# Kernel optimization log

Measured on AMD Instinct MI355X. Metric: run time of the kernel, lower is better.

The kernel has to match this reference:

```python
import jax, jax.numpy as jnp
import numpy as np

N = 100000
E = 1600000
IN_DIM = 128
HID = 64
NCOMM = 32


def setup_inputs() -> dict:
    key = jax.random.key(0)
    k = jax.random.split(key, 8)
    x = jax.random.normal(k[0], (N, IN_DIM), dtype=jnp.float32)
    edge_index = jax.random.randint(k[1], (2, E), 0, N, dtype=jnp.int64)
    s1 = 1.0 / np.sqrt(IN_DIM)
    s2 = 1.0 / np.sqrt(HID)
    W1 = jax.random.uniform(k[2], (IN_DIM, HID), jnp.float32, -s1, s1)
    b1 = jnp.zeros((HID,), jnp.float32)
    W2 = jax.random.uniform(k[3], (HID, HID), jnp.float32, -s2, s2)
    b2 = jnp.zeros((HID,), jnp.float32)
    Wfc = jax.random.uniform(k[4], (HID, NCOMM), jnp.float32, -s2, s2)
    bfc = jax.random.uniform(k[5], (NCOMM,), jnp.float32, -s2, s2)
    return {"x": x, "edge_index": edge_index, "W1": W1, "b1": b1,
            "W2": W2, "b2": b2, "Wfc": Wfc, "bfc": bfc}


def gcn_conv(x, row, col, norm, W, b):
    # PyG GCNConv: linear -> gather(source) * norm -> scatter_add(target) -> + bias
    h = x @ W                                    # [N, out]
    msgs = h[row] * norm[:, None]                # [E+N, out] gather (memory-bound)
    agg = jax.ops.segment_sum(msgs, col, num_segments=x.shape[0])
    return agg + b


def reference(x, edge_index, W1, b1, W2, b2, Wfc, bfc):
    n = x.shape[0]
    # add self-loops (PyG GCNConv default)
    loop = jnp.arange(n, dtype=edge_index.dtype)
    row = jnp.concatenate([edge_index[0], loop])  # source
    col = jnp.concatenate([edge_index[1], loop])  # target
    # symmetric normalization D^{-1/2} (A+I) D^{-1/2}
    deg = jax.ops.segment_sum(jnp.ones_like(col, dtype=x.dtype), col, num_segments=n)
    dinv = jnp.where(deg > 0, jax.lax.rsqrt(deg), 0.0)
    norm = dinv[row] * dinv[col]
    h = jax.nn.relu(gcn_conv(x, row, col, norm, W1, b1))   # dropout = identity (eval)
    h = jax.nn.relu(gcn_conv(h, row, col, norm, W2, b2))
    return jax.nn.sigmoid(h @ Wfc + bfc)
```

## Files before the change

### kernel.cpp

```cpp
#include <hip/hip_runtime.h>
#include <hip/hip_fp16.h>
#include <math.h>

#define N_NODES 100000
#define N_EDGES 1600000
#define IN_DIM  128
#define HID     64
#define NCOMM   32
#define NB        391
#define BSHIFT    8
#define EPB       4096
#define NBIN_BLK  391

typedef _Float16 f16x8 __attribute__((ext_vector_type(8)));
typedef float    f32x4 __attribute__((ext_vector_type(4)));

__global__ void k_detect(const unsigned int* __restrict__ e, int* __restrict__ flag) {
  int lane = threadIdx.x;
  unsigned v = 0;
  #pragma unroll
  for (int i = 0; i < 4; ++i) v |= e[2 * (lane * 4 + i) + 1];
  unsigned long long nz = __ballot(v != 0u);
  if (lane == 0) *flag = (nz == 0ull) ? 1 : 0;
}

__device__ __forceinline__ int load_idx(const int* e32, long long pos, int is64) {
  if (is64) return (int)(((const long long*)e32)[pos]);
  return e32[pos];
}

__global__ __launch_bounds__(256) void k_bhist(const int* __restrict__ e, int* __restrict__ bcnt,
                                               const int* __restrict__ flag) {
  __shared__ int cnt[NB];
  for (int i = threadIdx.x; i < NB; i += 256) cnt[i] = 0;
  __syncthreads();
  int is64 = *flag;
  long long base = (long long)blockIdx.x * EPB;
  #pragma unroll
  for (int j = 0; j < EPB / 256; ++j) {
    long long eid = base + j * 256 + threadIdx.x;
    if (eid < N_EDGES) {
      int c = load_idx(e, (long long)N_EDGES + eid, is64);
      atomicAdd(&cnt[c >> BSHIFT], 1);
    }
  }
  __syncthreads();
  for (int b = threadIdx.x; b < NB; b += 256)
    if (cnt[b]) atomicAdd(&bcnt[b], cnt[b]);
}

__global__ __launch_bounds__(512) void k_bscan(const int* __restrict__ bcnt, int* __restrict__ bptr,
                                               int* __restrict__ bcur) {
  __shared__ int sm[512];
  int t = threadIdx.x;
  int v = (t < NB) ? bcnt[t] : 0;
  sm[t] = v;
  __syncthreads();
  for (int off = 1; off < 512; off <<= 1) {
    int u = (t >= off) ? sm[t - off] : 0;
    __syncthreads();
    sm[t] += u;
    __syncthreads();
  }
  if (t < NB) {
    int ex = sm[t] - v;
    bptr[t] = ex;
    bcur[t] = ex;
  }
  if (t == 0) bptr[NB] = N_EDGES;
}

__global__ __launch_bounds__(256) void k_bin(const int* __restrict__ e, int* __restrict__ bcur,
                                             uint2* __restrict__ ebuf, const int* __restrict__ flag) {
  __shared__ int cnt[NB];
  __shared__ int base[NB];
  for (int i = threadIdx.x; i < NB; i += 256) cnt[i] = 0;
  __syncthreads();
  int is64 = *flag;
  long long eb = (long long)blockIdx.x * EPB;
  int rr[EPB / 256], cc[EPB / 256], lr[EPB / 256];
  #pragma unroll
  for (int j = 0; j < EPB / 256; ++j) {
    long long eid = eb + j * 256 + threadIdx.x;
    if (eid < N_EDGES) {
      rr[j] = load_idx(e, eid, is64);
      cc[j] = load_idx(e, (long long)N_EDGES + eid, is64);
      lr[j] = atomicAdd(&cnt[cc[j] >> BSHIFT], 1);
    }
  }
  __syncthreads();
  for (int b = threadIdx.x; b < NB; b += 256)
    base[b] = cnt[b] ? atomicAdd(&bcur[b], cnt[b]) : 0;
  __syncthreads();
  #pragma unroll
  for (int j = 0; j < EPB / 256; ++j) {
    long long eid = eb + j * 256 + threadIdx.x;
    if (eid < N_EDGES) {
      int pos = base[cc[j] >> BSHIFT] + lr[j];
      ebuf[pos] = make_uint2((unsigned)rr[j], (unsigned)cc[j]);
    }
  }
}

__global__ __launch_bounds__(256) void k_deg(const uint2* __restrict__ ebuf, const int* __restrict__ bptr,
                                             float* __restrict__ dinv, int* __restrict__ ptr) {
  __shared__ int cnt[256];
  __shared__ int scn[256];
  int t = threadIdx.x;
  int b = blockIdx.x;
  int c0 = b << BSHIFT;
  cnt[t] = 0;
  __syncthreads();
  int s = bptr[b], epos = bptr[b + 1];
  for (int i = s + t; i < epos; i += 256)
    atomicAdd(&cnt[(int)ebuf[i].y - c0], 1);
  __syncthreads();
  int d = cnt[t];
  scn[t] = d;
  __syncthreads();
  for (int off = 1; off < 256; off <<= 1) {
    int u = (t >= off) ? scn[t - off] : 0;
    __syncthreads();
    scn[t] += u;
    __syncthreads();
  }
  int node = c0 + t;
  if (node < N_NODES) {
    dinv[node] = rsqrtf((float)d + 1.0f);
    ptr[node] = bptr[b] + scn[t] - d;
  }
  if (b == NB - 1 && t == 0) ptr[N_NODES] = N_EDGES;
}

__global__ __launch_bounds__(1024) void k_fsort(const uint2* __restrict__ ebuf, const int* __restrict__ bptr,
                                                const int* __restrict__ ptr, const float* __restrict__ dinv,
                                                uint2* __restrict__ pk) {
  __shared__ int cur[256];
  int b = blockIdx.x;
  int c0 = b << BSHIFT;
  if (threadIdx.x < 256) {
    int node = c0 + threadIdx.x;
    cur[threadIdx.x] = (node < N_NODES) ? ptr[node] : 0;
  }
  __syncthreads();
  int s = bptr[b], epos = bptr[b + 1];
  for (int i = s + (int)threadIdx.x; i < epos; i += 1024) {
    uint2 ed = ebuf[i];
    int r = (int)ed.x, c = (int)ed.y;
    float w = dinv[r] * dinv[c];
    int pos = atomicAdd(&cur[c - c0], 1);
    pk[pos] = make_uint2((unsigned)r, __float_as_uint(w));
  }
}

template<int K, int M, bool FINAL, bool INH>
__global__ __launch_bounds__(256) void k_mfma(const void* __restrict__ X, const float* __restrict__ W,
                                              void* __restrict__ Y, const float* __restrict__ bias) {
  constexpr int NN = M / 16;
  constexpr int KS = K / 32;
  __shared__ char smem[M * K * 2];

  const int tid = threadIdx.x;
  for (int i = tid; i < K * M / 4; i += 256) {
    int k  = i / (M / 4);
    int mf = (i % (M / 4)) * 4;
    float4 wv = *(const float4*)(W + (size_t)k * M + mf);
    float wa[4] = {wv.x, wv.y, wv.z, wv.w};
    #pragma unroll
    for (int c = 0; c < 4; ++c) {
      int m = mf + c;
      int byte_off = m * (2 * K) + ((((k >> 3) << 4)) ^ ((m & 7) << 4)) + (k & 7) * 2;
      *(_Float16*)(smem + byte_off) = (_Float16)wa[c];
    }
  }
  __syncthreads();

  const int lane = tid & 63;
  const int wv_  = tid >> 6;
  const int rowbase = blockIdx.x * 128 + wv_ * 32;
  const int lr = lane & 15;
  const int kg = lane >> 4;
  const int r0 = rowbase + lr;
  const int r1 = r0 + 16;
  const int rc0 = (r0 < N_NODES) ? r0 : (N_NODES - 1);
  const int rc1 = (r1 < N_NODES) ? r1 : (N_NODES - 1);

  f32x4 acc[2][NN] = {};

  #pragma unroll
  for (int ks = 0; ks < KS; ++ks) {
    const int k0 = ks * 32 + kg * 8;
    f16x8 a0, a1;
    if constexpr (!INH) {
      const float* xr = (const float*)X;
      float4 u0 = *(const float4*)(xr + (size_t)rc0 * K + k0);
      float4 u1 = *(const float4*)(xr + (size_t)rc0 * K + k0 + 4);
      float4 u2 = *(const float4*)(xr + (size_t)rc1 * K + k0);
      float4 u3 = *(const float4*)(xr + (size_t)rc1 * K + k0 + 4);
      a0[0] = (_Float16)u0.x; a0[1] = (_Float16)u0.y; a0[2] = (_Float16)u0.z; a0[3] = (_Float16)u0.w;
      a0[4] = (_Float16)u1.x; a0[5] = (_Float16)u1.y; a0[6] = (_Float16)u1.z; a0[7] = (_Float16)u1.w;
      a1[0] = (_Float16)u2.x; a1[1] = (_Float16)u2.y; a1[2] = (_Float16)u2.z; a1[3] = (_Float16)u2.w;
      a1[4] = (_Float16)u3.x; a1[5] = (_Float16)u3.y; a1[6] = (_Float16)u3.z; a1[7] = (_Float16)u3.w;
    } else {
      const char* xb = (const char*)X;
      a0 = *(const f16x8*)(xb + (size_t)rc0 * (2 * K) + k0 * 2);
      a1 = *(const f16x8*)(xb + (size_t)rc1 * (2 * K) + k0 * 2);
    }
    const int slot = (k0 >> 3) << 4;
    #pragma unroll
    for (int n = 0; n < NN; ++n) {
      const int col = n * 16 + lr;
      f16x8 b = *(const f16x8*)(smem + col * (2 * K) + (slot ^ ((col & 7) << 4)));
      acc[0][n] = __builtin_amdgcn_mfma_f32_16x16x32_f16(a0, b, acc[0][n], 0, 0, 0);
      acc[1][n] = __builtin_amdgcn_mfma_f32_16x16x32_f16(a1, b, acc[1][n], 0, 0, 0);
    }
  }

  #pragma unroll
  for (int m2 = 0; m2 < 2; ++m2) {
    #pragma unroll
    for (int n = 0; n < NN; ++n) {
      const int col = n * 16 + lr;
      #pragma unroll
      for (int r = 0; r < 4; ++r) {
        const int row = rowbase + m2 * 16 + kg * 4 + r;
        if (row < N_NODES) {
          float v = acc[m2][n][r];
          if constexpr (FINAL) {
            v += bias[col];
            v = 1.f / (1.f + __expf(-v));
            ((float*)Y)[(size_t)row * M + col] = v;
          } else {
            ((__half*)Y)[(size_t)row * M + col] = __float2half(v);
          }
        }
      }
    }
  }
}

__device__ __forceinline__ void acc8(float* acc, uint4 h, float w) {
  __half2 p0 = *(__half2*)&h.x;
  __half2 p1 = *(__half2*)&h.y;
  __half2 p2 = *(__half2*)&h.z;
  __half2 p3 = *(__half2*)&h.w;
  float2 f0 = __half22float2(p0);
  float2 f1 = __half22float2(p1);
  float2 f2 = __half22float2(p2);
  float2 f3 = __half22float2(p3);
  acc[0] += f0.x * w; acc[1] += f0.y * w;
  acc[2] += f1.x * w; acc[3] += f1.y * w;
  acc[4] += f2.x * w; acc[5] += f2.y * w;
  acc[6] += f3.x * w; acc[7] += f3.y * w;
}

__global__ __launch_bounds__(256) void k_agg(const __half* __restrict__ H, __half* __restrict__ O,
                                             const int* __restrict__ ptr, const uint2* __restrict__ pk,
                                             const float* __restrict__ dinv, const float* __restrict__ bias) {
  int wid  = (blockIdx.x * 256 + threadIdx.x) >> 6;
  int lane = threadIdx.x & 63;
  if (wid >= N_NODES) return;
  const int q  = lane >> 3;
  const int fl = lane & 7;
  const char* Hb = (const char*)H;
  int s = ptr[wid], e = ptr[wid + 1];
  float acc[8] = {0.f, 0.f, 0.f, 0.f, 0.f, 0.f, 0.f, 0.f};
  for (int j = s; j < e; j += 16) {
    int i0 = j + q;
    int i1 = j + 8 + q;
    bool v0 = i0 < e;
    bool v1 = i1 < e;
    uint2 e0 = pk[v0 ? i0 : j];
    uint2 e1 = pk[v1 ? i1 : j];
    float w0 = v0 ? __uint_as_float(e0.y) : 0.f;
    float w1 = v1 ? __uint_as_float(e1.y) : 0.f;
    uint4 h0 = *(const uint4*)(Hb + (size_t)e0.x * (HID * 2) + fl * 16);
    uint4 h1 = *(const uint4*)(Hb + (size_t)e1.x * (HID * 2) + fl * 16);
    acc8(acc, h0, w0);
    acc8(acc, h1, w1);
  }
  if (q == 0) {
    float di = dinv[wid];
    uint4 hb = *(const uint4*)(Hb + (size_t)wid * (HID * 2) + fl * 16);
    acc8(acc, hb, di * di);
  }
  #pragma unroll
  for (int m = 8; m < 64; m <<= 1) {
    #pragma unroll
    for (int i = 0; i < 8; ++i) acc[i] += __shfl_xor(acc[i], m, 64);
  }
  if (lane < 8) {
    float4 ba = ((const float4*)bias)[2 * fl + 0];
    float4 bb = ((const float4*)bias)[2 * fl + 1];
    __half2 o0 = __floats2half2_rn(fmaxf(acc[0] + ba.x, 0.f), fmaxf(acc[1] + ba.y, 0.f));
    __half2 o1 = __floats2half2_rn(fmaxf(acc[2] + ba.z, 0.f), fmaxf(acc[3] + ba.w, 0.f));
    __half2 o2 = __floats2half2_rn(fmaxf(acc[4] + bb.x, 0.f), fmaxf(acc[5] + bb.y, 0.f));
    __half2 o3 = __floats2half2_rn(fmaxf(acc[6] + bb.z, 0.f), fmaxf(acc[7] + bb.w, 0.f));
    uint4 pv;
    pv.x = *(unsigned*)&o0;
    pv.y = *(unsigned*)&o1;
    pv.z = *(unsigned*)&o2;
    pv.w = *(unsigned*)&o3;
    *(uint4*)((char*)O + (size_t)wid * (HID * 2) + fl * 16) = pv;
  }
}

extern "C" void kernel_launch(void* const* d_in, const int* in_sizes, int n_in,
                              void* d_out, int out_size, void* d_ws, size_t ws_size,
                              hipStream_t stream) {
  const float* x   = (const float*)d_in[0];
  const int*   e   = (const int*)d_in[1];
  const float* W1  = (const float*)d_in[2];
  const float* b1  = (const float*)d_in[3];
  const float* W2  = (const float*)d_in[4];
  const float* b2  = (const float*)d_in[5];
  const float* Wfc = (const float*)d_in[6];
  const float* bfc = (const float*)d_in[7];
  float* out = (float*)d_out;

  char* ws = (char*)d_ws;
  __half* hbuf = (__half*)(ws);
  uint2*  ebuf = (uint2*) (ws);
  uint2*  pk   = (uint2*) (ws + 12800000);
  __half* abuf = (__half*)(ws + 25600000);
  float*  dinv = (float*) (ws + 38400000);
  int*    ptr  = (int*)   (ws + 38800000);
  int*    flag = (int*)   (ws + 39200064);
  int*    bcnt = (int*)   (ws + 39200128);
  int*    bptr = (int*)   (ws + 39201728);
  int*    bcur = (int*)   (ws + 39203392);

  hipMemsetAsync(bcnt, 0, NB * sizeof(int), stream);
  k_detect<<<1, 64, 0, stream>>>((const unsigned int*)e, flag);
  k_bhist<<<NBIN_BLK, 256, 0, stream>>>(e, bcnt, flag);
  k_bscan<<<1, 512, 0, stream>>>(bcnt, bptr, bcur);
  k_bin<<<NBIN_BLK, 256, 0, stream>>>(e, bcur, ebuf, flag);
  k_deg<<<NB, 256, 0, stream>>>(ebuf, bptr, dinv, ptr);
  k_fsort<<<NB, 1024, 0, stream>>>(ebuf, bptr, ptr, dinv, pk);

  const int gBlocks = (N_NODES + 127) / 128;
  k_mfma<IN_DIM, HID, false, false><<<gBlocks, 256, 0, stream>>>(x, W1, hbuf, nullptr);
  k_agg<<<N_NODES * 64 / 256, 256, 0, stream>>>(hbuf, abuf, ptr, pk, dinv, b1);
  k_mfma<HID, HID, false, true><<<gBlocks, 256, 0, stream>>>(abuf, W2, hbuf, nullptr);
  k_agg<<<N_NODES * 64 / 256, 256, 0, stream>>>(hbuf, abuf, ptr, pk, dinv, b2);
  k_mfma<HID, NCOMM, true, true><<<gBlocks, 256, 0, stream>>>(abuf, Wfc, out, bfc);
}
```

Before: 204.8 us.

## Factor GCN normalization into GEMM epilogue and fuse degree with CSR sort

The symmetric norm dinv[r]*dinv[c] is split: the GEMM epilogue scales each source row by dinv, and the aggregation scales the sum by the target's dinv. Aggregation therefore needs only source indices (4 bytes per edge instead of 8) and does plain adds, with a zeroed padding row at index N standing in for out-of-range edges. Degree counting and the within-bucket counting sort are fused into one kernel, and binned edges are packed into 32-bit words (17-bit row plus 8-bit local column). This removes a launch and the per-edge dinv gathers, and halves edge-list traffic. The trade-off is that fp16 features now carry the dinv scaling, which changes rounding slightly.

Result: no change. 203.8 us (-0.5%).

```diff
diff --git a/kernel.cpp b/kernel.cpp
--- a/kernel.cpp
+++ b/kernel.cpp
@@ -71,7 +71,7 @@
 }
 
 __global__ __launch_bounds__(256) void k_bin(const int* __restrict__ e, int* __restrict__ bcur,
-                                             uint2* __restrict__ ebuf, const int* __restrict__ flag) {
+                                             unsigned* __restrict__ ebuf, const int* __restrict__ flag) {
   __shared__ int cnt[NB];
   __shared__ int base[NB];
   for (int i = threadIdx.x; i < NB; i += 256) cnt[i] = 0;
@@ -97,15 +97,17 @@
     long long eid = eb + j * 256 + threadIdx.x;
     if (eid < N_EDGES) {
       int pos = base[cc[j] >> BSHIFT] + lr[j];
-      ebuf[pos] = make_uint2((unsigned)rr[j], (unsigned)cc[j]);
-    }
-  }
-}
-
-__global__ __launch_bounds__(256) void k_deg(const uint2* __restrict__ ebuf, const int* __restrict__ bptr,
-                                             float* __restrict__ dinv, int* __restrict__ ptr) {
+      ebuf[pos] = ((unsigned)(cc[j] & 255) << 17) | (unsigned)rr[j];
+    }
+  }
+}
+
+__global__ __launch_bounds__(256) void k_degsort(const unsigned* __restrict__ ebuf, const int* __restrict__ bptr,
+                                                 float* __restrict__ dinv, int* __restrict__ ptr,
+                                                 int* __restrict__ srow) {
   __shared__ int cnt[256];
   __shared__ int scn[256];
+  __shared__ int cur[256];
   int t = threadIdx.x;
   int b = blockIdx.x;
   int c0 = b << BSHIFT;
@@ -113,7 +115,7 @@
   __syncthreads();
   int s = bptr[b], epos = bptr[b + 1];
   for (int i = s + t; i < epos; i += 256)
-    atomicAdd(&cnt[(int)ebuf[i].y - c0], 1);
+    atomicAdd(&cnt[ebuf[i] >> 17], 1);
   __syncthreads();
   int d = cnt[t];
   scn[t] = d;
@@ -124,38 +126,26 @@
     scn[t] += u;
     __syncthreads();
   }
+  int myptr = s + scn[t] - d;
   int node = c0 + t;
   if (node < N_NODES) {
     dinv[node] = rsqrtf((float)d + 1.0f);
-    ptr[node] = bptr[b] + scn[t] - d;
+    ptr[node] = myptr;
+  }
+  cur[t] = myptr;
+  __syncthreads();
+  for (int i = s + t; i < epos; i += 256) {
+    unsigned w = ebuf[i];
+    int pos = atomicAdd(&cur[w >> 17], 1);
+    srow[pos] = (int)(w & 0x1FFFFu);
   }
   if (b == NB - 1 && t == 0) ptr[N_NODES] = N_EDGES;
-}
-
-__global__ __launch_bounds__(1024) void k_fsort(const uint2* __restrict__ ebuf, const int* __restrict__ bptr,
-                                                const int* __restrict__ ptr, const float* __restrict__ dinv,
-                                                uint2* __restrict__ pk) {
-  __shared__ int cur[256];
-  int b = blockIdx.x;
-  int c0 = b << BSHIFT;
-  if (threadIdx.x < 256) {
-    int node = c0 + threadIdx.x;
-    cur[threadIdx.x] = (node < N_NODES) ? ptr[node] : 0;
-  }
-  __syncthreads();
-  int s = bptr[b], epos = bptr[b + 1];
-  for (int i = s + (int)threadIdx.x; i < epos; i += 1024) {
-    uint2 ed = ebuf[i];
-    int r = (int)ed.x, c = (int)ed.y;
-    float w = dinv[r] * dinv[c];
-    int pos = atomicAdd(&cur[c - c0], 1);
-    pk[pos] = make_uint2((unsigned)r, __float_as_uint(w));
-  }
 }
 
 template<int K, int M, bool FINAL, bool INH>
 __global__ __launch_bounds__(256) void k_mfma(const void* __restrict__ X, const float* __restrict__ W,
-                                              void* __restrict__ Y, const float* __restrict__ bias) {
+                                              void* __restrict__ Y, const float* __restrict__ bias,
+                                              const float* __restrict__ dscale) {
   constexpr int NN = M / 16;
   constexpr int KS = K / 32;
   __shared__ char smem[M * K * 2];
@@ -219,19 +209,20 @@
   #pragma unroll
   for (int m2 = 0; m2 < 2; ++m2) {
     #pragma unroll
-    for (int n = 0; n < NN; ++n) {
-      const int col = n * 16 + lr;
-      #pragma unroll
-      for (int r = 0; r < 4; ++r) {
-        const int row = rowbase + m2 * 16 + kg * 4 + r;
-        if (row < N_NODES) {
+    for (int r = 0; r < 4; ++r) {
+      const int row = rowbase + m2 * 16 + kg * 4 + r;
+      if (row < N_NODES) {
+        float ds = FINAL ? 0.f : dscale[row];
+        #pragma unroll
+        for (int n = 0; n < NN; ++n) {
+          const int col = n * 16 + lr;
           float v = acc[m2][n][r];
           if constexpr (FINAL) {
             v += bias[col];
             v = 1.f / (1.f + __expf(-v));
             ((float*)Y)[(size_t)row * M + col] = v;
           } else {
-            ((__half*)Y)[(size_t)row * M + col] = __float2half(v);
+            ((__half*)Y)[(size_t)row * M + col] = __float2half(v * ds);
           }
         }
       }
@@ -239,7 +230,7 @@
   }
 }
 
-__device__ __forceinline__ void acc8(float* acc, uint4 h, float w) {
+__device__ __forceinline__ void addrow(float* acc, uint4 h) {
   __half2 p0 = *(__half2*)&h.x;
   __half2 p1 = *(__half2*)&h.y;
   __half2 p2 = *(__half2*)&h.z;
@@ -248,14 +239,14 @@
   float2 f1 = __half22float2(p1);
   float2 f2 = __half22float2(p2);
   float2 f3 = __half22float2(p3);
-  acc[0] += f0.x * w; acc[1] += f0.y * w;
-  acc[2] += f1.x * w; acc[3] += f1.y * w;
-  acc[4] += f2.x * w; acc[5] += f2.y * w;
-  acc[6] += f3.x * w; acc[7] += f3.y * w;
+  acc[0] += f0.x; acc[1] += f0.y;
+  acc[2] += f1.x; acc[3] += f1.y;
+  acc[4] += f2.x; acc[5] += f2.y;
+  acc[6] += f3.x; acc[7] += f3.y;
 }
 
 __global__ __launch_bounds__(256) void k_agg(const __half* __restrict__ H, __half* __restrict__ O,
-                                             const int* __restrict__ ptr, const uint2* __restrict__ pk,
+                                             const int* __restrict__ ptr, const int* __restrict__ srow,
                                              const float* __restrict__ dinv, const float* __restrict__ bias) {
   int wid  = (blockIdx.x * 256 + threadIdx.x) >> 6;
   int lane = threadIdx.x & 63;
@@ -268,21 +259,18 @@
   for (int j = s; j < e; j += 16) {
     int i0 = j + q;
     int i1 = j + 8 + q;
-    bool v0 = i0 < e;
-    bool v1 = i1 < e;
-    uint2 e0 = pk[v0 ? i0 : j];
-    uint2 e1 = pk[v1 ? i1 : j];
-    float w0 = v0 ? __uint_as_float(e0.y) : 0.f;
-    float w1 = v1 ? __uint_as_float(e1.y) : 0.f;
-    uint4 h0 = *(const uint4*)(Hb + (size_t)e0.x * (HID * 2) + fl * 16);
-    uint4 h1 = *(const uint4*)(Hb + (size_t)e1.x * (HID * 2) + fl * 16);
-    acc8(acc, h0, w0);
-    acc8(acc, h1, w1);
+    int r0 = srow[i0];
+    int r1 = srow[i1];
+    r0 = (i0 < e) ? r0 : N_NODES;
+    r1 = (i1 < e) ? r1 : N_NODES;
+    uint4 h0 = *(const uint4*)(Hb + (size_t)((unsigned)r0 * 128u + (unsigned)fl * 16u));
+    uint4 h1 = *(const uint4*)(Hb + (size_t)((unsigned)r1 * 128u + (unsigned)fl * 16u));
+    addrow(acc, h0);
+    addrow(acc, h1);
   }
   if (q == 0) {
-    float di = dinv[wid];
-    uint4 hb = *(const uint4*)(Hb + (size_t)wid * (HID * 2) + fl * 16);
-    acc8(acc, hb, di * di);
+    uint4 hb = *(const uint4*)(Hb + (size_t)((unsigned)wid * 128u + (unsigned)fl * 16u));
+    addrow(acc, hb);
   }
   #pragma unroll
   for (int m = 8; m < 64; m <<= 1) {
@@ -290,12 +278,13 @@
     for (int i = 0; i < 8; ++i) acc[i] += __shfl_xor(acc[i], m, 64);
   }
   if (lane < 8) {
+    float di = dinv[wid];
     float4 ba = ((const float4*)bias)[2 * fl + 0];
     float4 bb = ((const float4*)bias)[2 * fl + 1];
-    __half2 o0 = __floats2half2_rn(fmaxf(acc[0] + ba.x, 0.f), fmaxf(acc[1] + ba.y, 0.f));
-    __half2 o1 = __floats2half2_rn(fmaxf(acc[2] + ba.z, 0.f), fmaxf(acc[3] + ba.w, 0.f));
-    __half2 o2 = __floats2half2_rn(fmaxf(acc[4] + bb.x, 0.f), fmaxf(acc[5] + bb.y, 0.f));
-    __half2 o3 = __floats2half2_rn(fmaxf(acc[6] + bb.z, 0.f), fmaxf(acc[7] + bb.w, 0.f));
+    __half2 o0 = __floats2half2_rn(fmaxf(acc[0] * di + ba.x, 0.f), fmaxf(acc[1] * di + ba.y, 0.f));
+    __half2 o1 = __floats2half2_rn(fmaxf(acc[2] * di + ba.z, 0.f), fmaxf(acc[3] * di + ba.w, 0.f));
+    __half2 o2 = __floats2half2_rn(fmaxf(acc[4] * di + bb.x, 0.f), fmaxf(acc[5] * di + bb.y, 0.f));
+    __half2 o3 = __floats2half2_rn(fmaxf(acc[6] * di + bb.z, 0.f), fmaxf(acc[7] * di + bb.w, 0.f));
     uint4 pv;
     pv.x = *(unsigned*)&o0;
     pv.y = *(unsigned*)&o1;
@@ -319,29 +308,29 @@
   float* out = (float*)d_out;
 
   char* ws = (char*)d_ws;
-  __half* hbuf = (__half*)(ws);
-  uint2*  ebuf = (uint2*) (ws);
-  uint2*  pk   = (uint2*) (ws + 12800000);
-  __half* abuf = (__half*)(ws + 25600000);
-  float*  dinv = (float*) (ws + 38400000);
-  int*    ptr  = (int*)   (ws + 38800000);
-  int*    flag = (int*)   (ws + 39200064);
-  int*    bcnt = (int*)   (ws + 39200128);
-  int*    bptr = (int*)   (ws + 39201728);
-  int*    bcur = (int*)   (ws + 39203392);
+  __half*   hbuf = (__half*)  (ws);
+  unsigned* ebuf = (unsigned*)(ws);
+  int*      srow = (int*)     (ws + 12800256);
+  __half*   abuf = (__half*)  (ws + 19200320);
+  float*    dinv = (float*)   (ws + 32000320);
+  int*      ptr  = (int*)     (ws + 32400320);
+  int*      flag = (int*)     (ws + 32800384);
+  int*      bcnt = (int*)     (ws + 32800448);
+  int*      bptr = (int*)     (ws + 32802048);
+  int*      bcur = (int*)     (ws + 32803712);
 
   hipMemsetAsync(bcnt, 0, NB * sizeof(int), stream);
+  hipMemsetAsync(ws + (size_t)N_NODES * 128, 0, 128, stream);
   k_detect<<<1, 64, 0, stream>>>((const unsigned int*)e, flag);
   k_bhist<<<NBIN_BLK, 256, 0, stream>>>(e, bcnt, flag);
   k_bscan<<<1, 512, 0, stream>>>(bcnt, bptr, bcur);
   k_bin<<<NBIN_BLK, 256, 0, stream>>>(e, bcur, ebuf, flag);
-  k_deg<<<NB, 256, 0, stream>>>(ebuf, bptr, dinv, ptr);
-  k_fsort<<<NB, 1024, 0, stream>>>(ebuf, bptr, ptr, dinv, pk);
+  k_degsort<<<NB, 256, 0, stream>>>(ebuf, bptr, dinv, ptr, srow);
 
   const int gBlocks = (N_NODES + 127) / 128;
-  k_mfma<IN_DIM, HID, false, false><<<gBlocks, 256, 0, stream>>>(x, W1, hbuf, nullptr);
-  k_agg<<<N_NODES * 64 / 256, 256, 0, stream>>>(hbuf, abuf, ptr, pk, dinv, b1);
-  k_mfma<HID, HID, false, true><<<gBlocks, 256, 0, stream>>>(abuf, W2, hbuf, nullptr);
-  k_agg<<<N_NODES * 64 / 256, 256, 0, stream>>>(hbuf, abuf, ptr, pk, dinv, b2);
-  k_mfma<HID, NCOMM, true, true><<<gBlocks, 256, 0, stream>>>(abuf, Wfc, out, bfc);
-}
+  k_mfma<IN_DIM, HID, false, false><<<gBlocks, 256, 0, stream>>>(x, W1, hbuf, nullptr, dinv);
+  k_agg<<<N_NODES * 64 / 256, 256, 0, stream>>>(hbuf, abuf, ptr, srow, dinv, b1);
+  k_mfma<HID, HID, false, true><<<gBlocks, 256, 0, stream>>>(abuf, W2, hbuf, nullptr, dinv);
+  k_agg<<<N_NODES * 64 / 256, 256, 0, stream>>>(hbuf, abuf, ptr, srow, dinv, b2);
+  k_mfma<HID, NCOMM, true, true><<<gBlocks, 256, 0, stream>>>(abuf, Wfc, out, bfc, nullptr);
+}
```
